# Kernel tuning notes

Hardware: AMD Instinct MI355X
Metric: run time of the kernel (lower is better)

Reference implementation:

```python
import jax, jax.numpy as jnp
import numpy as np

B, T, D, H = 8, 512, 1024, 16
DK = D // H          # 64
S = 2 * T - 1        # 1023 relative positions


def setup_inputs() -> dict:
    key = jax.random.key(0)
    ks = jax.random.split(key, 10)
    s = 0.02
    return {
        "x": jax.random.normal(ks[0], (B, T, D), jnp.float32),
        "mask": jax.random.randint(ks[1], (B, T, T), 0, 2) > 0,
        "pos": jax.random.normal(ks[2], (1, S, D), jnp.float32),
        "Wqkv": jax.random.normal(ks[3], (3 * D, D), jnp.float32) * s,
        "bqkv": jnp.zeros((3 * D,), jnp.float32),
        "Wpos": jax.random.normal(ks[4], (D, D), jnp.float32) * s,
        "posu": jax.random.normal(ks[5], (1, 1, H, DK), jnp.float32) * s,
        "posv": jax.random.normal(ks[6], (1, 1, H, DK), jnp.float32) * s,
        "Wout": jax.random.normal(ks[7], (D, D), jnp.float32) * s,
        "bout": jnp.zeros((D,), jnp.float32),
    }


def reference(x, mask, pos, Wqkv, bqkv, Wpos, posu, posv, Wout, bout):
    # QKV projection and head split
    qkv = x @ Wqkv.T + bqkv                               # [B,T,3D]
    q, k, v = jnp.split(qkv, 3, axis=-1)
    q = q.reshape(B, T, H, DK)                            # [B,T,H,dk]
    k = k.reshape(B, T, H, DK).transpose(0, 2, 1, 3)      # [B,H,T,dk]
    v = v.reshape(B, T, H, DK).transpose(0, 2, 1, 3)      # [B,H,T,dk]
    # positional projection (no bias)
    p = (pos @ Wpos.T).reshape(1, S, H, DK).transpose(0, 2, 1, 3)  # [1,H,S,dk]
    # content (AC) and position (BD) terms
    q_u = (q + posu).transpose(0, 2, 1, 3)                # [B,H,T,dk]
    q_v = (q + posv).transpose(0, 2, 1, 3)                # [B,H,T,dk]
    AC = jnp.einsum('bhtd,bhsd->bhts', q_u, k)            # [B,H,T,T]
    matrix_bd = jnp.einsum('bhtd,zhsd->bhts', q_v, p)     # [B,H,T,S]
    # Transformer-XL style relative gather: index (j - i) + (T-1)
    r = jnp.arange(T)
    rel = (r[None, :] - r[:, None]) + (T - 1)             # [T,T], values in [0, S)
    BD = jnp.take_along_axis(matrix_bd, rel[None, None], axis=3)  # [B,H,T,T]
    scores = (AC + BD) / jnp.sqrt(jnp.float32(DK))
    scores = jnp.where(mask[:, None], scores, jnp.float32(-100000.0))
    weights = jax.nn.softmax(scores, axis=-1)             # [B,H,T,T]
    ctx = jnp.einsum('bhts,bhsd->bthd', weights, v).reshape(B, T, D)
    out = ctx @ Wout.T + bout                             # dropout rate 0 -> identity
    return out, weights
```

## Files before the change

### kernel.cpp

```cpp
#include <hip/hip_runtime.h>

#define BB 8
#define TT 512
#define DD 1024
#define HH 16
#define DKK 64
#define SS 1023

typedef unsigned short u16;
typedef __attribute__((ext_vector_type(8))) short bf16x8;
typedef __attribute__((ext_vector_type(4))) float f32x4;

#define MFMA16(a, b, c) __builtin_amdgcn_mfma_f32_16x16x32_bf16((a), (b), (c), 0, 0, 0)

#define WAVE_SYNC() do { asm volatile("s_waitcnt lgkmcnt(0)" ::: "memory"); __builtin_amdgcn_sched_barrier(0); } while (0)

__device__ __forceinline__ float us2f(u16 u) {
    unsigned int x = ((unsigned int)u) << 16;
    return __uint_as_float(x);
}
__device__ __forceinline__ u16 f2us(float f) {
    unsigned int x = __float_as_uint(f);
    unsigned int lsb = (x >> 16) & 1u;
    x += 0x7fffu + lsb;
    return (u16)(x >> 16);
}
__device__ __forceinline__ bf16x8 cvt8(const float* p) {
    float4 f1 = *(const float4*)p;
    float4 f2 = *(const float4*)(p + 4);
    bf16x8 r;
    r[0] = (short)f2us(f1.x); r[1] = (short)f2us(f1.y);
    r[2] = (short)f2us(f1.z); r[3] = (short)f2us(f1.w);
    r[4] = (short)f2us(f2.x); r[5] = (short)f2us(f2.y);
    r[6] = (short)f2us(f2.z); r[7] = (short)f2us(f2.w);
    return r;
}

__global__ void detect_kernel(const u16* __restrict__ w,
                              const unsigned int* __restrict__ mask,
                              int* __restrict__ flags) {
    if (threadIdx.x == 0 && blockIdx.x == 0) {
        int plaus = 0;
        for (int i = 0; i < 256; i++) {
            u16 hw = w[i];
            int e = (hw >> 7) & 0xFF;
            if (e == 0 || (e >= 87 && e <= 131)) plaus++;
        }
        flags[0] = (plaus >= 205) ? 1 : 0;
        int ok = 1;
        for (int i = 0; i < 64; i++) if (mask[i] > 1u) ok = 0;
        flags[1] = ok;
    }
}

__global__ __launch_bounds__(256) void pack_mask(const void* __restrict__ mask,
                                                 unsigned int* __restrict__ packed,
                                                 const int* __restrict__ flags) {
    const int idx = blockIdx.x * 256 + threadIdx.x;
    const int g = idx & 15;
    const size_t bt = (size_t)(idx >> 4);
    unsigned int bits = 0;
    if (flags[1]) {
        const int* mp = (const int*)mask + bt * TT + g;
        #pragma unroll
        for (int k = 0; k < 32; k++) if (mp[k * 16] != 0) bits |= (1u << k);
    } else {
        const signed char* mp = (const signed char*)mask + bt * TT + g;
        #pragma unroll
        for (int k = 0; k < 32; k++) if (mp[k * 16] != 0) bits |= (1u << k);
    }
    packed[idx] = bits;
}

template<int OMODE>
__global__ __launch_bounds__(256) void gemm_mfma(
    const void* __restrict__ Av, const void* __restrict__ Wv,
    const void* __restrict__ bias, const int* __restrict__ flags,
    float* __restrict__ qT, u16* __restrict__ kB, u16* __restrict__ vB,
    u16* __restrict__ pB, void* __restrict__ oout, int M, int N, int K)
{
    const bool isbf = (flags[0] != 0);
    __shared__ u16 As[64][40];
    __shared__ u16 Bs[64][40];
    const int tid = threadIdx.x;
    const int w = tid >> 6, lane = tid & 63;
    const int quad = lane >> 4, l16 = lane & 15;
    const int bn = blockIdx.x * 64, bm = blockIdx.y * 64;
    const int srow = tid >> 2;
    const int koff = (tid & 3) * 8;
    const int garow = (OMODE == 1) ? min(bm + srow, M - 1) : (bm + srow);
    const int gbrow = bn + srow;

    f32x4 C[4];
    #pragma unroll
    for (int i = 0; i < 4; i++) { C[i][0] = 0.f; C[i][1] = 0.f; C[i][2] = 0.f; C[i][3] = 0.f; }

    for (int k0 = 0; k0 < K; k0 += 32) {
        bf16x8 av, bv;
        if (OMODE == 2) {
            const int kk = k0 + koff;
            const float* ap = qT + (((size_t)((garow >> 9) * HH + (kk >> 6)) * TT + (garow & 511)) << 6) + (kk & 63);
            av = cvt8(ap);
        } else if (isbf) {
            av = *(const bf16x8*)((const u16*)Av + (size_t)garow * K + k0 + koff);
        } else {
            av = cvt8((const float*)Av + (size_t)garow * K + k0 + koff);
        }
        if (isbf) {
            bv = *(const bf16x8*)((const u16*)Wv + (size_t)gbrow * K + k0 + koff);
        } else {
            bv = cvt8((const float*)Wv + (size_t)gbrow * K + k0 + koff);
        }

        __syncthreads();
        *(bf16x8*)&As[srow][koff] = av;
        *(bf16x8*)&Bs[srow][koff] = bv;
        __syncthreads();

        bf16x8 af = *(const bf16x8*)&As[w * 16 + l16][quad * 8];
        #pragma unroll
        for (int ct = 0; ct < 4; ct++) {
            bf16x8 bf = *(const bf16x8*)&Bs[ct * 16 + l16][quad * 8];
            C[ct] = MFMA16(af, bf, C[ct]);
        }
    }

    #pragma unroll
    for (int ct = 0; ct < 4; ct++) {
        #pragma unroll
        for (int r = 0; r < 4; r++) {
            const int i = bm + w * 16 + quad * 4 + r;
            const int n = bn + ct * 16 + l16;
            float val = C[ct][r];
            if (OMODE == 0) {
                val += isbf ? us2f(((const u16*)bias)[n]) : ((const float*)bias)[n];
                const int sec = n >> 10, w_ = n & 1023;
                const int h_ = w_ >> 6, d_ = w_ & 63;
                const size_t bh_ = (size_t)((i >> 9) * HH + h_);
                const int t_ = i & 511;
                if (sec == 0) qT[((bh_ * TT + t_) << 6) + d_] = val;
                else if (sec == 1) kB[((bh_ * TT + t_) << 6) + d_] = f2us(val);
                else vB[((bh_ * DKK + d_) << 9) + t_] = f2us(val);
            } else if (OMODE == 1) {
                if (i < M) {
                    const int h_ = n >> 6, d_ = n & 63;
                    pB[((size_t)(h_ * 1024 + i) << 6) + d_] = f2us(val);
                }
            } else {
                val += isbf ? us2f(((const u16*)bias)[n]) : ((const float*)bias)[n];
                if (isbf) ((u16*)oout)[(size_t)i * N + n] = f2us(val);
                else ((float*)oout)[(size_t)i * N + n] = val;
            }
        }
    }
}

__global__ __launch_bounds__(256) void attn_mfma(
    float* __restrict__ qT, const u16* __restrict__ kB, const u16* __restrict__ vB,
    const u16* __restrict__ pB, const void* __restrict__ posu,
    const void* __restrict__ posv, const unsigned int* __restrict__ pmask,
    void* __restrict__ d_out, const int* __restrict__ flags)
{
    const int b = blockIdx.x;
    const int h = blockIdx.y;
    const int t0 = blockIdx.z << 6;
    const int tid = threadIdx.x;
    const int w = tid >> 6, lane = tid & 63;
    const int quad = lane >> 4, l16 = lane & 15;
    const bool isbf = (flags[0] != 0);
    const size_t bh = (size_t)b * HH + h;

    __shared__ u16 wls[4][16][268];
    u16* wme = &wls[w][0][0];
    float* bdw = (float*)wme;

    const int trow = t0 + w * 16 + quad * 4;
    unsigned int mrow[4];
    #pragma unroll
    for (int r = 0; r < 4; r++)
        mrow[r] = pmask[((size_t)(b * TT + trow + r) << 4) + l16];

    const int myrow = t0 + w * 16 + l16;
    const float* qrow = qT + ((bh * TT + myrow) << 6);
    bf16x8 aU[2], aV[2];
    #pragma unroll
    for (int f = 0; f < 2; f++) {
        const int d0 = f * 32 + quad * 8;
        float q8[8], pu8[8], pv8[8];
        *(float4*)&q8[0] = *(const float4*)(qrow + d0);
        *(float4*)&q8[4] = *(const float4*)(qrow + d0 + 4);
        if (isbf) {
            const u16* puP = (const u16*)posu + h * 64 + d0;
            const u16* pvP = (const u16*)posv + h * 64 + d0;
            #pragma unroll
            for (int j = 0; j < 8; j++) { pu8[j] = us2f(puP[j]); pv8[j] = us2f(pvP[j]); }
        } else {
            const float* puP = (const float*)posu + h * 64 + d0;
            const float* pvP = (const float*)posv + h * 64 + d0;
            #pragma unroll
            for (int j = 0; j < 8; j++) { pu8[j] = puP[j]; pv8[j] = pvP[j]; }
        }
        #pragma unroll
        for (int j = 0; j < 8; j++) {
            aU[f][j] = (short)f2us((q8[j] + pu8[j]) * 0.125f);
            aV[f][j] = (short)f2us((q8[j] + pv8[j]) * 0.125f);
        }
    }

    f32x4 S[32];
    #pragma unroll
    for (int ct = 0; ct < 32; ct++) { S[ct][0] = 0.f; S[ct][1] = 0.f; S[ct][2] = 0.f; S[ct][3] = 0.f; }
    const u16* kbase = kB + ((bh * TT) << 6) + quad * 8;
    #pragma unroll
    for (int ct = 0; ct < 32; ct++) {
        const u16* kp = kbase + ((size_t)(ct * 16 + l16) << 6);
        bf16x8 b0 = *(const bf16x8*)kp;
        bf16x8 b1 = *(const bf16x8*)(kp + 32);
        S[ct] = MFMA16(aU[0], b0, S[ct]);
        S[ct] = MFMA16(aU[1], b1, S[ct]);
    }

    const u16* pbaseh = pB + ((size_t)h << 16);
    for (int g = 0; g < 8; g++) {
        const int pb = g * 64 - t0 + 496 - w * 16;
        #pragma unroll
        for (int c5 = 0; c5 < 5; c5++) {
            const u16* pp = pbaseh + ((size_t)(pb + c5 * 16 + l16) << 6) + quad * 8;
            bf16x8 b0 = *(const bf16x8*)pp;
            bf16x8 b1 = *(const bf16x8*)(pp + 32);
            f32x4 c; c[0] = 0.f; c[1] = 0.f; c[2] = 0.f; c[3] = 0.f;
            c = MFMA16(aV[0], b0, c);
            c = MFMA16(aV[1], b1, c);
            #pragma unroll
            for (int r = 0; r < 4; r++)
                bdw[(quad * 4 + r) * 84 + c5 * 16 + l16] = c[r];
        }
        WAVE_SYNC();
        #pragma unroll
        for (int f = 0; f < 4; f++) {
            const int sc = f * 16 + l16;
            #pragma unroll
            for (int r = 0; r < 4; r++) {
                const int local = quad * 4 + r;
                S[g * 4 + f][r] += bdw[local * 83 + sc + 15];
            }
        }
    }

    #pragma unroll
    for (int ct = 0; ct < 32; ct++) {
        #pragma unroll
        for (int r = 0; r < 4; r++) {
            if (!(mrow[r] & (1u << ct))) S[ct][r] = -100000.0f;
        }
    }

    float mx[4] = {-3.0e38f, -3.0e38f, -3.0e38f, -3.0e38f};
    float sm[4] = {0.f, 0.f, 0.f, 0.f};
    #pragma unroll
    for (int ct = 0; ct < 32; ct++)
        #pragma unroll
        for (int r = 0; r < 4; r++) mx[r] = fmaxf(mx[r], S[ct][r]);
    #pragma unroll
    for (int r = 0; r < 4; r++)
        #pragma unroll
        for (int off = 1; off < 16; off <<= 1) mx[r] = fmaxf(mx[r], __shfl_xor(mx[r], off, 64));
    #pragma unroll
    for (int ct = 0; ct < 32; ct++)
        #pragma unroll
        for (int r = 0; r < 4; r++) {
            float e = __expf(S[ct][r] - mx[r]);
            S[ct][r] = e;
            sm[r] += e;
        }
    #pragma unroll
    for (int r = 0; r < 4; r++) {
        #pragma unroll
        for (int off = 1; off < 16; off <<= 1) sm[r] += __shfl_xor(sm[r], off, 64);
        sm[r] = 1.0f / sm[r];
    }

    f32x4 Cv[4];
    #pragma unroll
    for (int i = 0; i < 4; i++) { Cv[i][0] = 0.f; Cv[i][1] = 0.f; Cv[i][2] = 0.f; Cv[i][3] = 0.f; }
    const u16* vb0 = vB + ((bh * DKK) << 9) + quad * 8;
    const size_t wbase = (size_t)BB * TT * DD + (((bh * TT + trow)) << 9) + l16;

    #pragma unroll
    for (int p = 0; p < 2; p++) {
        #pragma unroll
        for (int cl = 0; cl < 16; cl++) {
            const int ct = p * 16 + cl;
            #pragma unroll
            for (int r = 0; r < 4; r++) {
                const float wv = S[ct][r] * sm[r];
                wls[w][quad * 4 + r][cl * 16 + l16] = f2us(wv);
                if (!isbf) ((float*)d_out)[wbase + ((size_t)r << 9) + ct * 16] = wv;
            }
        }
        WAVE_SYNC();
        if (isbf) {
            u16* wout = (u16*)d_out + (size_t)BB * TT * DD + ((bh * TT + t0 + w * 16) << 9) + p * 256;
            const int sr = lane >> 5, sc8 = (lane & 31) * 8;
            #pragma unroll
            for (int rr = 0; rr < 8; rr++) {
                bf16x8 vv = *(const bf16x8*)&wls[w][rr * 2 + sr][sc8];
                *(bf16x8*)(wout + ((size_t)(rr * 2 + sr) << 9) + sc8) = vv;
            }
        }
        #pragma unroll
        for (int kl = 0; kl < 8; kl++) {
            const int ks = p * 8 + kl;
            bf16x8 aw = *(const bf16x8*)&wls[w][l16][kl * 32 + quad * 8];
            #pragma unroll
            for (int ctd = 0; ctd < 4; ctd++) {
                const u16* vp = vb0 + ((size_t)(ctd * 16 + l16) << 9) + ks * 32;
                bf16x8 bv = *(const bf16x8*)vp;
                Cv[ctd] = MFMA16(aw, bv, Cv[ctd]);
            }
        }
        WAVE_SYNC();
    }

    float* crow = qT + ((bh * TT + trow) << 6) + l16;
    #pragma unroll
    for (int ctd = 0; ctd < 4; ctd++)
        #pragma unroll
        for (int r = 0; r < 4; r++)
            crow[(r << 6) + ctd * 16] = Cv[ctd][r];
}

extern "C" void kernel_launch(void* const* d_in, const int* in_sizes, int n_in,
                              void* d_out, int out_size, void* d_ws, size_t ws_size,
                              hipStream_t stream)
{
    const void* x    = d_in[0];
    const void* mask = d_in[1];
    const void* pos  = d_in[2];
    const void* Wqkv = d_in[3];
    const void* bqkv = d_in[4];
    const void* Wpos = d_in[5];
    const void* posu = d_in[6];
    const void* posv = d_in[7];
    const void* Wout = d_in[8];
    const void* bout = d_in[9];

    char* ws = (char*)d_ws;
    float* qT    = (float*)(ws + 0);
    u16*   kB    = (u16*)(ws + 16777216);
    u16*   vB    = (u16*)(ws + 25165824);
    u16*   pB    = (u16*)(ws + 33554432);
    int*   flags = (int*)(ws + 35651584);
    unsigned int* pmask = (unsigned int*)(ws + 35655680);

    detect_kernel<<<1, 64, 0, stream>>>((const u16*)Wqkv, (const unsigned int*)mask, flags);
    pack_mask<<<dim3(256), 256, 0, stream>>>(mask, pmask, flags);

    gemm_mfma<0><<<dim3(48, 64), 256, 0, stream>>>(
        x, Wqkv, bqkv, flags, qT, kB, vB, pB, nullptr, BB * TT, 3 * DD, DD);

    gemm_mfma<1><<<dim3(16, 16), 256, 0, stream>>>(
        pos, Wpos, nullptr, flags, qT, kB, vB, pB, nullptr, SS, DD, DD);

    attn_mfma<<<dim3(BB, HH, 8), 256, 0, stream>>>(
        qT, kB, vB, pB, posu, posv, pmask, d_out, flags);

    gemm_mfma<2><<<dim3(16, 64), 256, 0, stream>>>(
        nullptr, Wout, bout, flags, qT, kB, vB, pB, d_out, BB * TT, DD, DD);
}
```

Measured before the change: 496.0 us.

## Pre-convert operands to bf16 and use 128x128 GEMM tiles with direct LDS loads

Adds conversion kernels that turn x, pos and the weight matrices into bf16 buffers before the GEMMs run. The GEMM tile grows from 64x64 to 128x128, with 4x4 MFMA accumulators per wave, and operands are staged through global_load_lds instead of register round-trips. The attention kernel now writes the context directly as bf16 in [B,T,D] layout, so the output GEMM reads a plain row-major matrix. The aim is to raise data reuse and cut conversion work inside the GEMM loops. The cost is extra conversion launches and memory traffic, plus a non-pipelined load with a full vmcnt wait on every k-step.

```diff
diff --git a/kernel.cpp b/kernel.cpp
--- a/kernel.cpp
+++ b/kernel.cpp
@@ -35,6 +35,11 @@
     r[6] = (short)f2us(f2.z); r[7] = (short)f2us(f2.w);
     return r;
 }
+__device__ __forceinline__ void gload_lds16(const u16* g, u16* l) {
+    __builtin_amdgcn_global_load_lds(
+        (const __attribute__((address_space(1))) void*)g,
+        (__attribute__((address_space(3))) void*)l, 16, 0, 0);
+}
 
 __global__ void detect_kernel(const u16* __restrict__ w,
                               const unsigned int* __restrict__ mask,
@@ -72,94 +77,110 @@
     packed[idx] = bits;
 }
 
+__global__ __launch_bounds__(256) void cvt_bf16(const void* __restrict__ src,
+                                                u16* __restrict__ dst, int n8,
+                                                const int* __restrict__ flags) {
+    const bool isbf = (flags[0] != 0);
+    int i = blockIdx.x * 256 + threadIdx.x;
+    const int stride = gridDim.x * 256;
+    for (; i < n8; i += stride) {
+        if (isbf)
+            *(bf16x8*)(dst + (size_t)i * 8) = *(const bf16x8*)((const u16*)src + (size_t)i * 8);
+        else
+            *(bf16x8*)(dst + (size_t)i * 8) = cvt8((const float*)src + (size_t)i * 8);
+    }
+}
+
 template<int OMODE>
 __global__ __launch_bounds__(256) void gemm_mfma(
-    const void* __restrict__ Av, const void* __restrict__ Wv,
+    const u16* __restrict__ A, const u16* __restrict__ Bw,
     const void* __restrict__ bias, const int* __restrict__ flags,
     float* __restrict__ qT, u16* __restrict__ kB, u16* __restrict__ vB,
     u16* __restrict__ pB, void* __restrict__ oout, int M, int N, int K)
 {
     const bool isbf = (flags[0] != 0);
-    __shared__ u16 As[64][40];
-    __shared__ u16 Bs[64][40];
+    __shared__ u16 As[128 * 32];
+    __shared__ u16 Bs[128 * 32];
     const int tid = threadIdx.x;
     const int w = tid >> 6, lane = tid & 63;
     const int quad = lane >> 4, l16 = lane & 15;
-    const int bn = blockIdx.x * 64, bm = blockIdx.y * 64;
-    const int srow = tid >> 2;
-    const int koff = (tid & 3) * 8;
-    const int garow = (OMODE == 1) ? min(bm + srow, M - 1) : (bm + srow);
-    const int gbrow = bn + srow;
-
-    f32x4 C[4];
-    #pragma unroll
-    for (int i = 0; i < 4; i++) { C[i][0] = 0.f; C[i][1] = 0.f; C[i][2] = 0.f; C[i][3] = 0.f; }
+    const int wr = w >> 1, wc = w & 1;
+    const int bn = blockIdx.x * 128, bm = blockIdx.y * 128;
+    const int c0 = w * 2, c1 = w * 2 + 1;
+    const int sr0 = c0 * 16 + (lane >> 2);
+    const int sr1 = c1 * 16 + (lane >> 2);
+    const int skoff = (lane & 3) * 8;
+
+    f32x4 acc[4][4];
+    #pragma unroll
+    for (int m = 0; m < 4; m++)
+        #pragma unroll
+        for (int n = 0; n < 4; n++) {
+            acc[m][n][0] = 0.f; acc[m][n][1] = 0.f;
+            acc[m][n][2] = 0.f; acc[m][n][3] = 0.f;
+        }
 
     for (int k0 = 0; k0 < K; k0 += 32) {
-        bf16x8 av, bv;
-        if (OMODE == 2) {
-            const int kk = k0 + koff;
-            const float* ap = qT + (((size_t)((garow >> 9) * HH + (kk >> 6)) * TT + (garow & 511)) << 6) + (kk & 63);
-            av = cvt8(ap);
-        } else if (isbf) {
-            av = *(const bf16x8*)((const u16*)Av + (size_t)garow * K + k0 + koff);
-        } else {
-            av = cvt8((const float*)Av + (size_t)garow * K + k0 + koff);
-        }
-        if (isbf) {
-            bv = *(const bf16x8*)((const u16*)Wv + (size_t)gbrow * K + k0 + koff);
-        } else {
-            bv = cvt8((const float*)Wv + (size_t)gbrow * K + k0 + koff);
-        }
-
+        int ar0 = bm + sr0, ar1 = bm + sr1;
+        if (OMODE == 1) { ar0 = min(ar0, M - 1); ar1 = min(ar1, M - 1); }
         __syncthreads();
-        *(bf16x8*)&As[srow][koff] = av;
-        *(bf16x8*)&Bs[srow][koff] = bv;
+        gload_lds16(A + (size_t)ar0 * K + k0 + skoff, As + c0 * 512);
+        gload_lds16(A + (size_t)ar1 * K + k0 + skoff, As + c1 * 512);
+        gload_lds16(Bw + (size_t)(bn + sr0) * K + k0 + skoff, Bs + c0 * 512);
+        gload_lds16(Bw + (size_t)(bn + sr1) * K + k0 + skoff, Bs + c1 * 512);
+        asm volatile("s_waitcnt vmcnt(0)" ::: "memory");
         __syncthreads();
 
-        bf16x8 af = *(const bf16x8*)&As[w * 16 + l16][quad * 8];
-        #pragma unroll
-        for (int ct = 0; ct < 4; ct++) {
-            bf16x8 bf = *(const bf16x8*)&Bs[ct * 16 + l16][quad * 8];
-            C[ct] = MFMA16(af, bf, C[ct]);
-        }
-    }
-
-    #pragma unroll
-    for (int ct = 0; ct < 4; ct++) {
-        #pragma unroll
-        for (int r = 0; r < 4; r++) {
-            const int i = bm + w * 16 + quad * 4 + r;
-            const int n = bn + ct * 16 + l16;
-            float val = C[ct][r];
-            if (OMODE == 0) {
-                val += isbf ? us2f(((const u16*)bias)[n]) : ((const float*)bias)[n];
-                const int sec = n >> 10, w_ = n & 1023;
-                const int h_ = w_ >> 6, d_ = w_ & 63;
-                const size_t bh_ = (size_t)((i >> 9) * HH + h_);
-                const int t_ = i & 511;
-                if (sec == 0) qT[((bh_ * TT + t_) << 6) + d_] = val;
-                else if (sec == 1) kB[((bh_ * TT + t_) << 6) + d_] = f2us(val);
-                else vB[((bh_ * DKK + d_) << 9) + t_] = f2us(val);
-            } else if (OMODE == 1) {
-                if (i < M) {
-                    const int h_ = n >> 6, d_ = n & 63;
-                    pB[((size_t)(h_ * 1024 + i) << 6) + d_] = f2us(val);
+        bf16x8 af[4], bfr[4];
+        #pragma unroll
+        for (int m = 0; m < 4; m++)
+            af[m] = *(const bf16x8*)&As[(wr * 64 + m * 16 + l16) * 32 + quad * 8];
+        #pragma unroll
+        for (int n = 0; n < 4; n++)
+            bfr[n] = *(const bf16x8*)&Bs[(wc * 64 + n * 16 + l16) * 32 + quad * 8];
+        #pragma unroll
+        for (int m = 0; m < 4; m++)
+            #pragma unroll
+            for (int n = 0; n < 4; n++)
+                acc[m][n] = MFMA16(af[m], bfr[n], acc[m][n]);
+    }
+
+    #pragma unroll
+    for (int m = 0; m < 4; m++)
+        #pragma unroll
+        for (int nn = 0; nn < 4; nn++)
+            #pragma unroll
+            for (int rr = 0; rr < 4; rr++) {
+                const int i = bm + wr * 64 + m * 16 + quad * 4 + rr;
+                const int n = bn + wc * 64 + nn * 16 + l16;
+                float val = acc[m][nn][rr];
+                if (OMODE == 0) {
+                    val += isbf ? us2f(((const u16*)bias)[n]) : ((const float*)bias)[n];
+                    const int sec = n >> 10, w_ = n & 1023;
+                    const int h_ = w_ >> 6, d_ = w_ & 63;
+                    const size_t bh_ = (size_t)((i >> 9) * HH + h_);
+                    const int t_ = i & 511;
+                    if (sec == 0) qT[((bh_ * TT + t_) << 6) + d_] = val;
+                    else if (sec == 1) kB[((bh_ * TT + t_) << 6) + d_] = f2us(val);
+                    else vB[((bh_ * DKK + d_) << 9) + t_] = f2us(val);
+                } else if (OMODE == 1) {
+                    if (i < M) {
+                        const int h_ = n >> 6, d_ = n & 63;
+                        pB[((size_t)(h_ * 1024 + i) << 6) + d_] = f2us(val);
+                    }
+                } else {
+                    val += isbf ? us2f(((const u16*)bias)[n]) : ((const float*)bias)[n];
+                    if (isbf) ((u16*)oout)[(size_t)i * N + n] = f2us(val);
+                    else ((float*)oout)[(size_t)i * N + n] = val;
                 }
-            } else {
-                val += isbf ? us2f(((const u16*)bias)[n]) : ((const float*)bias)[n];
-                if (isbf) ((u16*)oout)[(size_t)i * N + n] = f2us(val);
-                else ((float*)oout)[(size_t)i * N + n] = val;
             }
-        }
-    }
 }
 
 __global__ __launch_bounds__(256) void attn_mfma(
     float* __restrict__ qT, const u16* __restrict__ kB, const u16* __restrict__ vB,
     const u16* __restrict__ pB, const void* __restrict__ posu,
     const void* __restrict__ posv, const unsigned int* __restrict__ pmask,
-    void* __restrict__ d_out, const int* __restrict__ flags)
+    void* __restrict__ d_out, u16* __restrict__ ctxB, const int* __restrict__ flags)
 {
     const int b = blockIdx.x;
     const int h = blockIdx.y;
@@ -322,12 +343,12 @@
         WAVE_SYNC();
     }
 
-    float* crow = qT + ((bh * TT + trow) << 6) + l16;
+    u16* crow = ctxB + ((size_t)(b * TT + trow) << 10) + h * 64 + l16;
     #pragma unroll
     for (int ctd = 0; ctd < 4; ctd++)
         #pragma unroll
         for (int r = 0; r < 4; r++)
-            crow[(r << 6) + ctd * 16] = Cv[ctd][r];
+            crow[((size_t)r << 10) + ctd * 16] = f2us(Cv[ctd][r]);
 }
 
 extern "C" void kernel_launch(void* const* d_in, const int* in_sizes, int n_in,
@@ -352,19 +373,31 @@
     u16*   pB    = (u16*)(ws + 33554432);
     int*   flags = (int*)(ws + 35651584);
     unsigned int* pmask = (unsigned int*)(ws + 35655680);
+    u16*   xB    = (u16*)(ws + 35917824);
+    u16*   WqkvB = (u16*)(ws + 44306432);
+    u16*   WposB = (u16*)(ws + 50597888);
+    u16*   posB  = (u16*)(ws + 52695040);
+    u16*   WoutB = (u16*)(ws + 54792192);
+    u16*   ctxB  = xB;
 
     detect_kernel<<<1, 64, 0, stream>>>((const u16*)Wqkv, (const unsigned int*)mask, flags);
     pack_mask<<<dim3(256), 256, 0, stream>>>(mask, pmask, flags);
 
-    gemm_mfma<0><<<dim3(48, 64), 256, 0, stream>>>(
-        x, Wqkv, bqkv, flags, qT, kB, vB, pB, nullptr, BB * TT, 3 * DD, DD);
-
-    gemm_mfma<1><<<dim3(16, 16), 256, 0, stream>>>(
-        pos, Wpos, nullptr, flags, qT, kB, vB, pB, nullptr, SS, DD, DD);
+    cvt_bf16<<<dim3(1024), 256, 0, stream>>>(x,    xB,    4096 * 1024 / 8, flags);
+    cvt_bf16<<<dim3(1024), 256, 0, stream>>>(Wqkv, WqkvB, 3072 * 1024 / 8, flags);
+    cvt_bf16<<<dim3(512),  256, 0, stream>>>(Wpos, WposB, 1024 * 1024 / 8, flags);
+    cvt_bf16<<<dim3(512),  256, 0, stream>>>(pos,  posB,  1023 * 1024 / 8, flags);
+    cvt_bf16<<<dim3(512),  256, 0, stream>>>(Wout, WoutB, 1024 * 1024 / 8, flags);
+
+    gemm_mfma<0><<<dim3(24, 32), 256, 0, stream>>>(
+        xB, WqkvB, bqkv, flags, qT, kB, vB, pB, nullptr, BB * TT, 3 * DD, DD);
+
+    gemm_mfma<1><<<dim3(8, 8), 256, 0, stream>>>(
+        posB, WposB, nullptr, flags, qT, kB, vB, pB, nullptr, SS, DD, DD);
 
     attn_mfma<<<dim3(BB, HH, 8), 256, 0, stream>>>(
-        qT, kB, vB, pB, posu, posv, pmask, d_out, flags);
-
-    gemm_mfma<2><<<dim3(16, 64), 256, 0, stream>>>(
-        nullptr, Wout, bout, flags, qT, kB, vB, pB, d_out, BB * TT, DD, DD);
-}
+        qT, kB, vB, pB, posu, posv, pmask, d_out, ctxB, flags);
+
+    gemm_mfma<2><<<dim3(8, 32), 256, 0, stream>>>(
+        ctxB, WoutB, bout, flags, qT, kB, vB, pB, d_out, BB * TT, DD, DD);
+}
```

Result: faster. 442.7 us (-10.8%).
